# Optimization experiments

Hardware: AMD Instinct MI355X
Metric: run time of the kernel (lower is better)

The kernel has to match this reference:

```python
import jax, jax.numpy as jnp
import numpy as np
from jax import lax

VOCAB = 32000
D = 256      # d_model
N = 16       # n_neurons
NL = 6       # n_layers
DS = 16      # d_state
DC = 4       # d_conv
DI = 512     # d_inner = expand * d_model
DTR = 16     # dt_rank = ceil(D/16)
NH = 4       # attention heads
HD = D // NH
B, L = 1, 128


def setup_inputs() -> dict:
    key = jax.random.key(0)
    ks = list(jax.random.split(key, 32))
    it = iter(ks)

    def rn(shape, scale):
        return jax.random.normal(next(it), shape, jnp.float32) * scale

    p = {}
    p["x"] = jax.random.randint(next(it), (B, L), 0, VOCAB, dtype=jnp.int32)
    p["embedding"] = rn((VOCAB, D), 0.02)
    p["norm1_w"] = jnp.ones((NL, D)); p["norm1_b"] = jnp.zeros((NL, D))
    p["norm2_w"] = jnp.ones((NL, D)); p["norm2_b"] = jnp.zeros((NL, D))
    # Mamba params (stacked over layers)
    p["in_proj_w"] = rn((NL, 2 * DI, D), D ** -0.5)
    p["conv_w"] = rn((NL, DI, DC), DC ** -0.5)
    p["conv_b"] = jnp.zeros((NL, DI))
    p["x_proj_w"] = rn((NL, DTR + 2 * DS, DI), DI ** -0.5)
    p["dt_proj_w"] = rn((NL, DI, DTR), DTR ** -0.5)
    dt0 = jax.random.uniform(next(it), (NL, DI), jnp.float32, 1e-3, 1e-1)
    p["dt_proj_b"] = jnp.log(jnp.expm1(dt0))  # inverse softplus init
    p["A_log"] = jnp.log(jnp.tile(jnp.arange(1.0, DS + 1.0, dtype=jnp.float32), (NL, DI, 1)))
    p["skip_D"] = jnp.ones((NL, DI))
    p["out_proj_w"] = rn((NL, D, DI), DI ** -0.5)
    # cross-neuron MHA params
    p["attn_in_w"] = rn((NL, 3 * D, D), D ** -0.5)
    p["attn_in_b"] = jnp.zeros((NL, 3 * D))
    p["attn_out_w"] = rn((NL, D, D), D ** -0.5)
    p["attn_out_b"] = jnp.zeros((NL, D))
    p["norm_f_w"] = jnp.ones((D,)); p["norm_f_b"] = jnp.zeros((D,))
    p["head_b"] = jnp.zeros((VOCAB,))
    return p


def _ln(x, w, b):
    m = x.mean(-1, keepdims=True)
    v = ((x - m) ** 2).mean(-1, keepdims=True)
    return (x - m) * lax.rsqrt(v + 1e-5) * w + b


def _mamba(x, ipw, cw, cb, xpw, dpw, dpb, alog, dskip, opw):
    # x: (BN, L, D)
    BN, Ls, _ = x.shape
    xz = x @ ipw.T                       # (BN, L, 2*DI)
    u, z = xz[..., :DI], xz[..., DI:]
    # depthwise causal conv1d, kernel DC, left-pad DC-1
    uc = lax.conv_general_dilated(
        u.swapaxes(1, 2), cw[:, None, :], (1,), [(DC - 1, 0)],
        dimension_numbers=("NCH", "OIH", "NCH"), feature_group_count=DI)
    u = jax.nn.silu(uc + cb[None, :, None]).swapaxes(1, 2)  # (BN, L, DI)
    xdbl = u @ xpw.T                     # (BN, L, DTR+2*DS)
    dt = jax.nn.softplus(xdbl[..., :DTR] @ dpw.T + dpb)     # (BN, L, DI)
    Bm = xdbl[..., DTR:DTR + DS]
    Cm = xdbl[..., DTR + DS:]
    A = -jnp.exp(alog)                   # (DI, DS)

    def step(h, ins):
        dt_t, b_t, c_t, u_t = ins        # (BN,DI) (BN,DS) (BN,DS) (BN,DI)
        h = jnp.exp(dt_t[..., None] * A) * h + (dt_t * u_t)[..., None] * b_t[:, None, :]
        return h, jnp.einsum("bds,bs->bd", h, c_t)

    h0 = jnp.zeros((BN, DI, DS), x.dtype)
    _, ys = lax.scan(step, h0, (dt.swapaxes(0, 1), Bm.swapaxes(0, 1),
                                Cm.swapaxes(0, 1), u.swapaxes(0, 1)))
    y = ys.swapaxes(0, 1) + u * dskip
    return (y * jax.nn.silu(z)) @ opw.T


def _mha(x, iw, ib, ow, ob):
    # x: (B*L, N, D); self-attention across neurons
    Bq, S, _ = x.shape
    qkv = x @ iw.T + ib
    q, k, v = jnp.split(qkv, 3, axis=-1)
    q = q.reshape(Bq, S, NH, HD); k = k.reshape(Bq, S, NH, HD); v = v.reshape(Bq, S, NH, HD)
    att = jax.nn.softmax(jnp.einsum("bqhd,bkhd->bhqk", q, k) / np.float32(np.sqrt(HD)), axis=-1)
    o = jnp.einsum("bhqk,bkhd->bqhd", att, v).reshape(Bq, S, D)
    return o @ ow.T + ob


def reference(x, embedding, norm1_w, norm1_b, norm2_w, norm2_b, in_proj_w, conv_w,
              conv_b, x_proj_w, dt_proj_w, dt_proj_b, A_log, skip_D, out_proj_w,
              attn_in_w, attn_in_b, attn_out_w, attn_out_b, norm_f_w, norm_f_b, head_b):
    Bb, Ll = x.shape
    h = embedding[x]                                             # (B, L, D)
    h = jnp.broadcast_to(h[:, None], (Bb, N, Ll, D)).reshape(Bb * N, Ll, D)
    for i in range(NL):
        h = h + _mamba(_ln(h, norm1_w[i], norm1_b[i]), in_proj_w[i], conv_w[i],
                       conv_b[i], x_proj_w[i], dt_proj_w[i], dt_proj_b[i],
                       A_log[i], skip_D[i], out_proj_w[i])
        xc = _ln(h, norm2_w[i], norm2_b[i]).reshape(Bb, N, Ll, D)
        xc = xc.transpose(0, 2, 1, 3).reshape(Bb * Ll, N, D)
        co = _mha(xc, attn_in_w[i], attn_in_b[i], attn_out_w[i], attn_out_b[i])
        h = h + co.reshape(Bb, Ll, N, D).transpose(0, 2, 1, 3).reshape(Bb * N, Ll, D)
    h = h.reshape(Bb, N, Ll, D).mean(axis=1)                     # avg over neurons
    return _ln(h, norm_f_w, norm_f_b) @ embedding.T + head_b     # tied head
```

## Files before the change

kernel.cpp:

```cpp
#include <hip/hip_runtime.h>
#include <hip/hip_bf16.h>

typedef __bf16 bf16x8 __attribute__((ext_vector_type(8)));
typedef float f32x4 __attribute__((ext_vector_type(4)));

constexpr int SEQ    = 128;
constexpr int NVOCAB = 32000;

constexpr size_t O_HA = 0;
constexpr size_t O_HB = O_HA + (size_t)SEQ*256;
constexpr size_t O_U  = O_HB + (size_t)SEQ*256;
constexpr size_t O_DT = O_U  + (size_t)SEQ*512;
constexpr size_t O_ZS = O_DT + (size_t)SEQ*512;
constexpr size_t O_BC = O_ZS + (size_t)SEQ*512;
constexpr size_t O_YG = O_BC + (size_t)SEQ*32;
constexpr size_t O_AH = O_YG + (size_t)SEQ*512;
constexpr size_t O_EB = O_AH + (size_t)SEQ*256;

__device__ __forceinline__ float wsum(float p) {
    #pragma unroll
    for (int m = 1; m < 64; m <<= 1) p += __shfl_xor(p, m);
    return p;
}
__device__ __forceinline__ float dot4(float4 a, float4 b) {
    return a.x*b.x + a.y*b.y + a.z*b.z + a.w*b.w;
}

template<int MR, int KK>
__device__ __forceinline__ void gemmT(
    const float* __restrict__ Wg, const float* __restrict__ A, int AS,
    float* __restrict__ pb, float* __restrict__ dest, int DS,
    const float* __restrict__ addsrc, int ASS, const float* __restrict__ bias)
{
    const int tid  = threadIdx.x;
    const int lane = tid & 63;
    const int wv   = tid >> 6;
    const int kg   = wv >> 2;
    const int cg   = wv & 3;
    const int tq = lane & 3, cs = lane >> 2;
    const int c0 = cg*64 + cs*4;
    constexpr int KH  = KK/2;
    constexpr int NCH = KH/16;
    const int kb = kg*KH;
    const float* W0 = Wg + (size_t)(c0+0)*KK + kb + tq*4;
    const float* W1 = Wg + (size_t)(c0+1)*KK + kb + tq*4;
    const float* W2 = Wg + (size_t)(c0+2)*KK + kb + tq*4;
    const float* W3 = Wg + (size_t)(c0+3)*KK + kb + tq*4;

    float acc[MR][4];
    #pragma unroll
    for (int r = 0; r < MR; ++r)
        #pragma unroll
        for (int j = 0; j < 4; ++j) acc[r][j] = 0.0f;

    float4 e0 = *(const float4*)(W0);
    float4 e1 = *(const float4*)(W1);
    float4 e2 = *(const float4*)(W2);
    float4 e3 = *(const float4*)(W3);
    float4 o0, o1, o2, o3;

    #pragma unroll
    for (int ch = 0; ch < NCH; ch += 2) {
        o0 = *(const float4*)(W0 + (ch+1)*16);
        o1 = *(const float4*)(W1 + (ch+1)*16);
        o2 = *(const float4*)(W2 + (ch+1)*16);
        o3 = *(const float4*)(W3 + (ch+1)*16);
        #pragma unroll
        for (int r = 0; r < MR; ++r) {
            float4 a = *(const float4*)&A[r*AS + kb + ch*16 + tq*4];
            acc[r][0] += dot4(a, e0);
            acc[r][1] += dot4(a, e1);
            acc[r][2] += dot4(a, e2);
            acc[r][3] += dot4(a, e3);
        }
        if (ch + 2 < NCH) {
            e0 = *(const float4*)(W0 + (ch+2)*16);
            e1 = *(const float4*)(W1 + (ch+2)*16);
            e2 = *(const float4*)(W2 + (ch+2)*16);
            e3 = *(const float4*)(W3 + (ch+2)*16);
        }
        #pragma unroll
        for (int r = 0; r < MR; ++r) {
            float4 a = *(const float4*)&A[r*AS + kb + (ch+1)*16 + tq*4];
            acc[r][0] += dot4(a, o0);
            acc[r][1] += dot4(a, o1);
            acc[r][2] += dot4(a, o2);
            acc[r][3] += dot4(a, o3);
        }
    }
    #pragma unroll
    for (int r = 0; r < MR; ++r)
        #pragma unroll
        for (int j = 0; j < 4; ++j) {
            float v = acc[r][j];
            v += __shfl_xor(v, 1);
            v += __shfl_xor(v, 2);
            acc[r][j] = v;
        }
    if (tq == 0) {
        #pragma unroll
        for (int r = 0; r < MR; ++r)
            #pragma unroll
            for (int j = 0; j < 4; ++j)
                pb[(kg*MR + r)*256 + c0 + j] = acc[r][j];
    }
    __syncthreads();
    if (tid < 256) {
        int c = tid;
        #pragma unroll
        for (int r = 0; r < MR; ++r) {
            float v = pb[r*256 + c] + pb[(MR + r)*256 + c];
            if (bias)   v += bias[c];
            if (addsrc) v += addsrc[r*ASS + c];
            dest[r*DS + c] = v;
        }
    }
}

__device__ __forceinline__ void ln_row(const float* __restrict__ src, float* __restrict__ dst,
                                       const float* __restrict__ w, const float* __restrict__ b)
{
    int lane = threadIdx.x & 63;
    float4 x = *(const float4*)&src[lane*4];
    float sm = wsum(x.x + x.y + x.z + x.w);
    float mean = sm * (1.0f/256.0f);
    float d0 = x.x-mean, d1 = x.y-mean, d2 = x.z-mean, d3 = x.w-mean;
    float var = wsum(d0*d0 + d1*d1 + d2*d2 + d3*d3) * (1.0f/256.0f);
    float rstd = rsqrtf(var + 1e-5f);
    float4 ww = *(const float4*)&w[lane*4];
    float4 bb = *(const float4*)&b[lane*4];
    float4 o;
    o.x = d0*rstd*ww.x + bb.x;
    o.y = d1*rstd*ww.y + bb.y;
    o.z = d2*rstd*ww.z + bb.z;
    o.w = d3*rstd*ww.w + bb.w;
    *(float4*)&dst[lane*4] = o;
}

__global__ __launch_bounds__(256) void cvt_emb_kernel(const float* __restrict__ e,
                                                      __hip_bfloat16* __restrict__ o)
{
    size_t base = (size_t)(blockIdx.x * 256 + threadIdx.x) * 16;
    #pragma unroll
    for (int j = 0; j < 16; j += 4) {
        float4 v = *(const float4*)&e[base + j];
        o[base + j + 0] = __float2bfloat16(v.x);
        o[base + j + 1] = __float2bfloat16(v.y);
        o[base + j + 2] = __float2bfloat16(v.z);
        o[base + j + 3] = __float2bfloat16(v.w);
    }
}

__global__ __launch_bounds__(512) void rowk_kernel(
    const int* __restrict__ x, const float* __restrict__ emb,
    const float* __restrict__ n1w_l, const float* __restrict__ n1b_l,
    const float* __restrict__ n2w_l, const float* __restrict__ n2b_l,
    const float* __restrict__ ipw_l, const float* __restrict__ cw_l, const float* __restrict__ cb_l,
    const float* __restrict__ xpw_l, const float* __restrict__ dpw_l, const float* __restrict__ dpb_l,
    const float* __restrict__ opw_l, const float* __restrict__ aivw_l, const float* __restrict__ aivb_l,
    const float* __restrict__ aow_l, const float* __restrict__ aob_l,
    const float* __restrict__ nfw, const float* __restrict__ nfb,
    const float* __restrict__ hin, float* __restrict__ hout,
    const float* __restrict__ ygv, float* __restrict__ uv, float* __restrict__ dtv,
    float* __restrict__ zsv, float* __restrict__ bcv, __hip_bfloat16* __restrict__ AHb,
    int li)
{
    __shared__ float SM[8384];
    float* hP  = SM;
    float* h1  = SM + 1056;
    float* sLN = SM + 2112;
    float* sAX = SM + 3168;
    float* zR  = SM + 5248;
    float* suR = SM + 5760;
    float* sxR = SM + 6272;
    float* pb  = SM + 6336;

    const int r = blockIdx.x;
    const int tid = threadIdx.x;
    const int lane = tid & 63, wv = tid >> 6;
    int rr[4];
    #pragma unroll
    for (int j = 0; j < 4; ++j) { int v = r - 3 + j; rr[j] = v < 0 ? 0 : v; }

    #pragma unroll
    for (int j = 0; j < 2; ++j) {
        int idx = j*512 + tid;
        int hr = idx >> 8, hc = idx & 255;
        if (li <= 1) hP[hr*264 + hc] = emb[(size_t)x[rr[hr]]*256 + hc];
        else         hP[hr*264 + hc] = hin[rr[hr]*256 + hc];
    }
    __syncthreads();

    float* hC = hP;
    if (li >= 1) {
        #pragma unroll
        for (int j = 0; j < 4; ++j)
            sAX[j*520 + tid] = ygv[rr[j]*512 + tid];
        __syncthreads();
        gemmT<4,512>(opw_l, sAX, 520, pb, h1, 264, hP, 264, nullptr);
        __syncthreads();
        if (wv < 4) ln_row(h1 + wv*264, sLN + wv*264, n2w_l, n2b_l);
        __syncthreads();
        gemmT<4,256>(aivw_l, sLN, 264, pb, sAX, 520, nullptr, 0, aivb_l);
        __syncthreads();
        gemmT<4,256>(aow_l, sAX, 520, pb, h1, 264, h1, 264, aob_l);
        __syncthreads();
        hC = h1;
        if (tid < 256) hout[r*256 + tid] = h1[3*264 + tid];
        if (li == 6) {
            if (tid < 256) {
                float v = h1[3*264 + tid];
                float s = wsum(v);
                float q = wsum(v*v);
                if (lane == 0) { sxR[wv] = s; sxR[8 + wv] = q; }
            }
            __syncthreads();
            if (tid < 256) {
                float v = h1[3*264 + tid];
                float mean = (sxR[0]+sxR[1]+sxR[2]+sxR[3]) * (1.0f/256.0f);
                float var  = (sxR[8]+sxR[9]+sxR[10]+sxR[11]) * (1.0f/256.0f) - mean*mean;
                float rstd = rsqrtf(var + 1e-5f);
                AHb[r*256 + tid] = __float2bfloat16((v - mean)*rstd*nfw[tid] + nfb[tid]);
            }
            return;
        }
    }

    if (wv < 4) ln_row(hC + wv*264, sLN + wv*264, n1w_l, n1b_l);
    __syncthreads();
    gemmT<4,256>(ipw_l,                   sLN, 264, pb, sAX,       520, nullptr, 0, nullptr);
    __syncthreads();
    gemmT<4,256>(ipw_l + (size_t)256*256, sLN, 264, pb, sAX + 256, 520, nullptr, 0, nullptr);
    __syncthreads();
    gemmT<1,256>(ipw_l + (size_t)512*256, sLN + 3*264, 264, pb, zR,       512, nullptr, 0, nullptr);
    __syncthreads();
    gemmT<1,256>(ipw_l + (size_t)768*256, sLN + 3*264, 264, pb, zR + 256, 512, nullptr, 0, nullptr);
    __syncthreads();

    {
        int d = tid;
        float4 c4 = *(const float4*)&cw_l[d*4];
        float acc = cb_l[d];
        if (r >= 3) acc += sAX[d]        * c4.x;
        if (r >= 2) acc += sAX[520 + d]  * c4.y;
        if (r >= 1) acc += sAX[1040 + d] * c4.z;
        acc += sAX[1560 + d] * c4.w;
        float sg = acc / (1.0f + __expf(-acc));
        suR[d] = sg;
        uv[r*512 + d] = sg;
        float z = zR[d];
        zsv[r*512 + d] = z / (1.0f + __expf(-z));
    }
    __syncthreads();

    {
        float4 a0 = *(const float4*)&suR[lane*4];
        float4 a1 = *(const float4*)&suR[256 + lane*4];
        float p[6];
        #pragma unroll
        for (int j = 0; j < 6; ++j) {
            int c = wv*6 + j;
            float4 q0 = *(const float4*)&xpw_l[(size_t)c*512 + lane*4];
            float4 q1 = *(const float4*)&xpw_l[(size_t)c*512 + 256 + lane*4];
            p[j] = dot4(a0, q0) + dot4(a1, q1);
        }
        #pragma unroll
        for (int m = 1; m < 64; m <<= 1) {
            #pragma unroll
            for (int j = 0; j < 6; ++j) p[j] += __shfl_xor(p[j], m);
        }
        if (lane == 0) {
            #pragma unroll
            for (int j = 0; j < 6; ++j) sxR[wv*6 + j] = p[j];
        }
    }
    __syncthreads();
    if (tid >= 16 && tid < 48) bcv[r*32 + tid - 16] = sxR[tid];

    {
        int d = tid;
        float4 sx0 = *(const float4*)&sxR[0];
        float4 sx1 = *(const float4*)&sxR[4];
        float4 sx2 = *(const float4*)&sxR[8];
        float4 sx3 = *(const float4*)&sxR[12];
        const float4* dp = (const float4*)&dpw_l[(size_t)d*16];
        float acc = dpb_l[d] + dot4(dp[0], sx0) + dot4(dp[1], sx1)
                             + dot4(dp[2], sx2) + dot4(dp[3], sx3);
        dtv[r*512 + d] = fmaxf(acc, 0.0f) + log1pf(__expf(-fabsf(acc)));
    }
}

__global__ __launch_bounds__(256) void scan_kernel(
    const float* __restrict__ dt, const float* __restrict__ u, const float* __restrict__ zs,
    const float* __restrict__ bcv,
    const float* __restrict__ alog_l, const float* __restrict__ dsk_l,
    float* __restrict__ yg)
{
    __shared__ float s5[5*128];
    float* sdt = s5;        float* su2 = s5 + 128;
    float* sz2 = s5 + 256;  float* sB  = s5 + 384;  float* sC = s5 + 512;
    int tid = threadIdx.x;
    int s  = tid & 15, dl = tid >> 4;
    int d0 = blockIdx.x * 16;
    int d  = d0 + dl;
    float a_ds = -__expf(alog_l[d*16 + s]);
    float dskv = dsk_l[d];
    float hst = 0.0f;
    for (int t0 = 0; t0 < SEQ; t0 += 8) {
        __syncthreads();
        if (tid < 128) {
            int tt = tid >> 4, j = tid & 15;
            int t = t0 + tt;
            sdt[tt*16+j] = dt[t*512 + d0 + j];
            su2[tt*16+j] = u [t*512 + d0 + j];
            sz2[tt*16+j] = zs[t*512 + d0 + j];
        } else {
            int q = tid - 128;
            int tt = q >> 4, j = q & 15;
            int t = t0 + tt;
            sB[tt*16+j] = bcv[t*32 + j];
            sC[tt*16+j] = bcv[t*32 + 16 + j];
        }
        __syncthreads();
        #pragma unroll
        for (int tt = 0; tt < 8; ++tt) {
            float dtvv = sdt[tt*16+dl];
            float uvv  = su2[tt*16+dl];
            hst = __expf(dtvv * a_ds) * hst + dtvv * uvv * sB[tt*16+s];
            float p = hst * sC[tt*16+s];
            p += __shfl_xor(p, 1);
            p += __shfl_xor(p, 2);
            p += __shfl_xor(p, 4);
            p += __shfl_xor(p, 8);
            if (s == 0) {
                float y = p + uvv * dskv;
                yg[(t0+tt)*512 + d] = y * sz2[tt*16+dl];
            }
        }
    }
}

__global__ __launch_bounds__(256) void head_mfma_kernel(
    const __hip_bfloat16* __restrict__ AHb, const __hip_bfloat16* __restrict__ Eb,
    const float* __restrict__ hb, float* __restrict__ out)
{
    int tid = threadIdx.x;
    int lane = tid & 63;
    int wv = tid >> 6;
    int mbase = blockIdx.y * 16;
    int nbase = blockIdx.x * 64 + wv * 16;
    int m = mbase + (lane & 15);
    int n = nbase + (lane & 15);
    int k0 = (lane >> 4) * 8;
    const __bf16* Ap = (const __bf16*)AHb + m*256 + k0;
    const __bf16* Bp = (const __bf16*)Eb + (size_t)n*256 + k0;
    f32x4 acc = {0.0f, 0.0f, 0.0f, 0.0f};
    #pragma unroll
    for (int kb = 0; kb < 256; kb += 32) {
        bf16x8 a  = *(const bf16x8*)(Ap + kb);
        bf16x8 bb = *(const bf16x8*)(Bp + kb);
        acc = __builtin_amdgcn_mfma_f32_16x16x32_bf16(a, bb, acc, 0, 0, 0);
    }
    int col = lane & 15;
    int rq = lane >> 4;
    float bias = hb[nbase + col];
    #pragma unroll
    for (int i = 0; i < 4; ++i)
        out[(size_t)(mbase + rq*4 + i)*NVOCAB + nbase + col] = acc[i] + bias;
}

extern "C" void kernel_launch(void* const* d_in, const int* in_sizes, int n_in,
                              void* d_out, int out_size, void* d_ws, size_t ws_size,
                              hipStream_t stream)
{
    const int*   xin = (const int*)d_in[0];
    const float* emb = (const float*)d_in[1];
    const float* n1w = (const float*)d_in[2];
    const float* n1b = (const float*)d_in[3];
    const float* n2w = (const float*)d_in[4];
    const float* n2b = (const float*)d_in[5];
    const float* ipw = (const float*)d_in[6];
    const float* cw  = (const float*)d_in[7];
    const float* cb  = (const float*)d_in[8];
    const float* xpw = (const float*)d_in[9];
    const float* dpw = (const float*)d_in[10];
    const float* dpb = (const float*)d_in[11];
    const float* alog= (const float*)d_in[12];
    const float* dsk = (const float*)d_in[13];
    const float* opw = (const float*)d_in[14];
    const float* aiw = (const float*)d_in[15];
    const float* aib = (const float*)d_in[16];
    const float* aow = (const float*)d_in[17];
    const float* aob = (const float*)d_in[18];
    const float* nfw = (const float*)d_in[19];
    const float* nfb = (const float*)d_in[20];
    const float* hb  = (const float*)d_in[21];
    float* ws  = (float*)d_ws;
    float* out = (float*)d_out;

    __hip_bfloat16* AHb = (__hip_bfloat16*)(ws + O_AH);
    __hip_bfloat16* Eb  = (__hip_bfloat16*)(ws + O_EB);

    cvt_emb_kernel<<<2000, 256, 0, stream>>>(emb, Eb);

    for (int i = 0; i <= 6; ++i) {
        int ka = i <= 5 ? i : 5;
        int kc = i >= 1 ? i - 1 : 0;
        const float* hin  = (i % 2 == 0) ? ws + O_HA : ws + O_HB;
        float*       hout = (i % 2 == 0) ? ws + O_HB : ws + O_HA;
        rowk_kernel<<<128, 512, 0, stream>>>(
            xin, emb,
            n1w + ka*256, n1b + ka*256,
            n2w + kc*256, n2b + kc*256,
            ipw + (size_t)ka*1024*256, cw + (size_t)ka*512*4, cb + ka*512,
            xpw + (size_t)ka*48*512, dpw + (size_t)ka*512*16, dpb + ka*512,
            opw + (size_t)kc*256*512,
            aiw + (size_t)kc*768*256 + (size_t)512*256, aib + kc*768 + 512,
            aow + (size_t)kc*256*256, aob + kc*256,
            nfw, nfb,
            hin, hout,
            ws + O_YG, ws + O_U, ws + O_DT, ws + O_ZS, ws + O_BC, AHb,
            i);
        if (i <= 5)
            scan_kernel<<<32, 256, 0, stream>>>(
                ws + O_DT, ws + O_U, ws + O_ZS, ws + O_BC,
                alog + (size_t)i*512*16, dsk + i*512, ws + O_YG);
    }
    head_mfma_kernel<<<dim3(NVOCAB/64, SEQ/16), 256, 0, stream>>>(AHb, Eb, hb, out);
}
```

Before: 671.1 us.

## Convert per-row layer GEMMs to bf16 MFMA with pre-converted weights

Result: faster. 601.4 us (-10.4%).

```diff
diff --git a/kernel.cpp b/kernel.cpp
--- a/kernel.cpp
+++ b/kernel.cpp
@@ -3,6 +3,7 @@
 
 typedef __bf16 bf16x8 __attribute__((ext_vector_type(8)));
 typedef float f32x4 __attribute__((ext_vector_type(4)));
+typedef __hip_bfloat16 hbf;
 
 constexpr int SEQ    = 128;
 constexpr int NVOCAB = 32000;
@@ -16,6 +17,10 @@
 constexpr size_t O_YG = O_BC + (size_t)SEQ*32;
 constexpr size_t O_AH = O_YG + (size_t)SEQ*512;
 constexpr size_t O_EB = O_AH + (size_t)SEQ*256;
+constexpr size_t O_WIP= O_EB + (size_t)NVOCAB*256/2;
+constexpr size_t O_WOP= O_WIP+ (size_t)6*1024*256/2;
+constexpr size_t O_WAV= O_WOP+ (size_t)6*256*512/2;
+constexpr size_t O_WAO= O_WAV+ (size_t)6*256*256/2;
 
 __device__ __forceinline__ float wsum(float p) {
     #pragma unroll
@@ -26,99 +31,54 @@
     return a.x*b.x + a.y*b.y + a.z*b.z + a.w*b.w;
 }
 
-template<int MR, int KK>
-__device__ __forceinline__ void gemmT(
-    const float* __restrict__ Wg, const float* __restrict__ A, int AS,
-    float* __restrict__ pb, float* __restrict__ dest, int DS,
+template<int KK, int NT, bool R3>
+__device__ __forceinline__ void gemmM(
+    const hbf* __restrict__ Wb, const hbf* __restrict__ Ab, int ASb,
+    float* __restrict__ dest, int DS, hbf* __restrict__ destb, int DSB,
     const float* __restrict__ addsrc, int ASS, const float* __restrict__ bias)
 {
-    const int tid  = threadIdx.x;
-    const int lane = tid & 63;
-    const int wv   = tid >> 6;
-    const int kg   = wv >> 2;
-    const int cg   = wv & 3;
-    const int tq = lane & 3, cs = lane >> 2;
-    const int c0 = cg*64 + cs*4;
-    constexpr int KH  = KK/2;
-    constexpr int NCH = KH/16;
-    const int kb = kg*KH;
-    const float* W0 = Wg + (size_t)(c0+0)*KK + kb + tq*4;
-    const float* W1 = Wg + (size_t)(c0+1)*KK + kb + tq*4;
-    const float* W2 = Wg + (size_t)(c0+2)*KK + kb + tq*4;
-    const float* W3 = Wg + (size_t)(c0+3)*KK + kb + tq*4;
-
-    float acc[MR][4];
-    #pragma unroll
-    for (int r = 0; r < MR; ++r)
-        #pragma unroll
-        for (int j = 0; j < 4; ++j) acc[r][j] = 0.0f;
-
-    float4 e0 = *(const float4*)(W0);
-    float4 e1 = *(const float4*)(W1);
-    float4 e2 = *(const float4*)(W2);
-    float4 e3 = *(const float4*)(W3);
-    float4 o0, o1, o2, o3;
-
-    #pragma unroll
-    for (int ch = 0; ch < NCH; ch += 2) {
-        o0 = *(const float4*)(W0 + (ch+1)*16);
-        o1 = *(const float4*)(W1 + (ch+1)*16);
-        o2 = *(const float4*)(W2 + (ch+1)*16);
-        o3 = *(const float4*)(W3 + (ch+1)*16);
-        #pragma unroll
-        for (int r = 0; r < MR; ++r) {
-            float4 a = *(const float4*)&A[r*AS + kb + ch*16 + tq*4];
-            acc[r][0] += dot4(a, e0);
-            acc[r][1] += dot4(a, e1);
-            acc[r][2] += dot4(a, e2);
-            acc[r][3] += dot4(a, e3);
-        }
-        if (ch + 2 < NCH) {
-            e0 = *(const float4*)(W0 + (ch+2)*16);
-            e1 = *(const float4*)(W1 + (ch+2)*16);
-            e2 = *(const float4*)(W2 + (ch+2)*16);
-            e3 = *(const float4*)(W3 + (ch+2)*16);
-        }
-        #pragma unroll
-        for (int r = 0; r < MR; ++r) {
-            float4 a = *(const float4*)&A[r*AS + kb + (ch+1)*16 + tq*4];
-            acc[r][0] += dot4(a, o0);
-            acc[r][1] += dot4(a, o1);
-            acc[r][2] += dot4(a, o2);
-            acc[r][3] += dot4(a, o3);
-        }
-    }
-    #pragma unroll
-    for (int r = 0; r < MR; ++r)
-        #pragma unroll
-        for (int j = 0; j < 4; ++j) {
-            float v = acc[r][j];
-            v += __shfl_xor(v, 1);
-            v += __shfl_xor(v, 2);
-            acc[r][j] = v;
-        }
-    if (tq == 0) {
-        #pragma unroll
-        for (int r = 0; r < MR; ++r)
+    constexpr int TPW = NT/128;
+    constexpr int NCH = KK/32;
+    const int lane = threadIdx.x & 63;
+    const int wv   = threadIdx.x >> 6;
+    const int col  = lane & 15;
+    const int kq   = lane >> 4;
+    const __bf16* Ap = (const __bf16*)Ab + (lane & 3)*ASb + kq*8;
+    const __bf16* Wp = (const __bf16*)Wb + (size_t)(wv*TPW*16 + col)*KK + kq*8;
+    f32x4 acc[TPW];
+    #pragma unroll
+    for (int t = 0; t < TPW; ++t) acc[t] = (f32x4){0.f,0.f,0.f,0.f};
+    #pragma unroll
+    for (int ch = 0; ch < NCH; ++ch) {
+        bf16x8 a = *(const bf16x8*)(Ap + ch*32);
+        #pragma unroll
+        for (int t = 0; t < TPW; ++t) {
+            bf16x8 b = *(const bf16x8*)(Wp + (size_t)t*16*KK + ch*32);
+            acc[t] = __builtin_amdgcn_mfma_f32_16x16x32_bf16(a, b, acc[t], 0, 0, 0);
+        }
+    }
+    if (lane < 16) {
+        #pragma unroll
+        for (int t = 0; t < TPW; ++t) {
+            int c = (wv*TPW + t)*16 + col;
+            float bv = bias ? bias[c] : 0.0f;
             #pragma unroll
-            for (int j = 0; j < 4; ++j)
-                pb[(kg*MR + r)*256 + c0 + j] = acc[r][j];
-    }
-    __syncthreads();
-    if (tid < 256) {
-        int c = tid;
-        #pragma unroll
-        for (int r = 0; r < MR; ++r) {
-            float v = pb[r*256 + c] + pb[(MR + r)*256 + c];
-            if (bias)   v += bias[c];
-            if (addsrc) v += addsrc[r*ASS + c];
-            dest[r*DS + c] = v;
-        }
-    }
-}
-
-__device__ __forceinline__ void ln_row(const float* __restrict__ src, float* __restrict__ dst,
-                                       const float* __restrict__ w, const float* __restrict__ b)
+            for (int i = 0; i < 4; ++i) {
+                float v = acc[t][i] + bv;
+                if (addsrc) v += addsrc[i*ASS + c];
+                if (R3) {
+                    if (i == 3) dest[c] = v;
+                } else {
+                    if (dest)  dest[i*DS + c] = v;
+                    if (destb) destb[i*DSB + c] = __float2bfloat16(v);
+                }
+            }
+        }
+    }
+}
+
+__device__ __forceinline__ void ln_row_b(const float* __restrict__ src, hbf* __restrict__ dstb,
+                                         const float* __restrict__ w, const float* __restrict__ b)
 {
     int lane = threadIdx.x & 63;
     float4 x = *(const float4*)&src[lane*4];
@@ -129,16 +89,14 @@
     float rstd = rsqrtf(var + 1e-5f);
     float4 ww = *(const float4*)&w[lane*4];
     float4 bb = *(const float4*)&b[lane*4];
-    float4 o;
-    o.x = d0*rstd*ww.x + bb.x;
-    o.y = d1*rstd*ww.y + bb.y;
-    o.z = d2*rstd*ww.z + bb.z;
-    o.w = d3*rstd*ww.w + bb.w;
-    *(float4*)&dst[lane*4] = o;
+    dstb[lane*4+0] = __float2bfloat16(d0*rstd*ww.x + bb.x);
+    dstb[lane*4+1] = __float2bfloat16(d1*rstd*ww.y + bb.y);
+    dstb[lane*4+2] = __float2bfloat16(d2*rstd*ww.z + bb.z);
+    dstb[lane*4+3] = __float2bfloat16(d3*rstd*ww.w + bb.w);
 }
 
 __global__ __launch_bounds__(256) void cvt_emb_kernel(const float* __restrict__ e,
-                                                      __hip_bfloat16* __restrict__ o)
+                                                      hbf* __restrict__ o)
 {
     size_t base = (size_t)(blockIdx.x * 256 + threadIdx.x) * 16;
     #pragma unroll
@@ -151,29 +109,49 @@
     }
 }
 
+__global__ __launch_bounds__(256) void cvt_w_kernel(
+    const float* __restrict__ ipw, const float* __restrict__ opw,
+    const float* __restrict__ aiw, const float* __restrict__ aow,
+    float* __restrict__ ws)
+{
+    hbf* dip = (hbf*)(ws + O_WIP);
+    hbf* dop = (hbf*)(ws + O_WOP);
+    hbf* dav = (hbf*)(ws + O_WAV);
+    hbf* dao = (hbf*)(ws + O_WAO);
+    int tid = blockIdx.x * 256 + threadIdx.x;
+    int stride = gridDim.x * 256;
+    for (int i = tid; i < 6*1024*256; i += stride) dip[i] = __float2bfloat16(ipw[i]);
+    for (int i = tid; i < 6*256*512;  i += stride) dop[i] = __float2bfloat16(opw[i]);
+    for (int i = tid; i < 6*256*256;  i += stride)
+        dav[i] = __float2bfloat16(aiw[(size_t)(i >> 16)*768*256 + 512*256 + (i & 65535)]);
+    for (int i = tid; i < 6*256*256;  i += stride) dao[i] = __float2bfloat16(aow[i]);
+}
+
 __global__ __launch_bounds__(512) void rowk_kernel(
     const int* __restrict__ x, const float* __restrict__ emb,
     const float* __restrict__ n1w_l, const float* __restrict__ n1b_l,
     const float* __restrict__ n2w_l, const float* __restrict__ n2b_l,
-    const float* __restrict__ ipw_l, const float* __restrict__ cw_l, const float* __restrict__ cb_l,
+    const hbf* __restrict__ ipb_l, const float* __restrict__ cw_l, const float* __restrict__ cb_l,
     const float* __restrict__ xpw_l, const float* __restrict__ dpw_l, const float* __restrict__ dpb_l,
-    const float* __restrict__ opw_l, const float* __restrict__ aivw_l, const float* __restrict__ aivb_l,
-    const float* __restrict__ aow_l, const float* __restrict__ aob_l,
+    const hbf* __restrict__ opb_l, const hbf* __restrict__ avb_l, const float* __restrict__ aivb_l,
+    const hbf* __restrict__ aob_wl, const float* __restrict__ aob_l,
     const float* __restrict__ nfw, const float* __restrict__ nfb,
     const float* __restrict__ hin, float* __restrict__ hout,
     const float* __restrict__ ygv, float* __restrict__ uv, float* __restrict__ dtv,
-    float* __restrict__ zsv, float* __restrict__ bcv, __hip_bfloat16* __restrict__ AHb,
+    float* __restrict__ zsv, float* __restrict__ bcv, hbf* __restrict__ AHb,
     int li)
 {
-    __shared__ float SM[8384];
+    __shared__ float SM[5280];
     float* hP  = SM;
     float* h1  = SM + 1056;
-    float* sLN = SM + 2112;
-    float* sAX = SM + 3168;
-    float* zR  = SM + 5248;
-    float* suR = SM + 5760;
-    float* sxR = SM + 6272;
-    float* pb  = SM + 6336;
+    float* sAX = SM + 2112;
+    float* zR  = SM + 4192;
+    float* suR = SM + 4704;
+    float* sxR = SM + 5216;
+    __shared__ __align__(16) hbf SB[4192];
+    hbf* sYb  = SB;
+    hbf* sLNb = SB + 2080;
+    hbf* sVb  = SB + 3136;
 
     const int r = blockIdx.x;
     const int tid = threadIdx.x;
@@ -195,15 +173,15 @@
     if (li >= 1) {
         #pragma unroll
         for (int j = 0; j < 4; ++j)
-            sAX[j*520 + tid] = ygv[rr[j]*512 + tid];
-        __syncthreads();
-        gemmT<4,512>(opw_l, sAX, 520, pb, h1, 264, hP, 264, nullptr);
-        __syncthreads();
-        if (wv < 4) ln_row(h1 + wv*264, sLN + wv*264, n2w_l, n2b_l);
-        __syncthreads();
-        gemmT<4,256>(aivw_l, sLN, 264, pb, sAX, 520, nullptr, 0, aivb_l);
-        __syncthreads();
-        gemmT<4,256>(aow_l, sAX, 520, pb, h1, 264, h1, 264, aob_l);
+            sYb[j*520 + tid] = __float2bfloat16(ygv[rr[j]*512 + tid]);
+        __syncthreads();
+        gemmM<512,256,false>(opb_l, sYb, 520, h1, 264, nullptr, 0, hP, 264, nullptr);
+        __syncthreads();
+        if (wv < 4) ln_row_b(h1 + wv*264, sLNb + wv*264, n2w_l, n2b_l);
+        __syncthreads();
+        gemmM<256,256,false>(avb_l, sLNb, 264, nullptr, 0, sVb, 264, nullptr, 0, aivb_l);
+        __syncthreads();
+        gemmM<256,256,false>(aob_wl, sVb, 264, h1, 264, nullptr, 0, h1, 264, aob_l);
         __syncthreads();
         hC = h1;
         if (tid < 256) hout[r*256 + tid] = h1[3*264 + tid];
@@ -226,15 +204,10 @@
         }
     }
 
-    if (wv < 4) ln_row(hC + wv*264, sLN + wv*264, n1w_l, n1b_l);
+    if (wv < 4) ln_row_b(hC + wv*264, sLNb + wv*264, n1w_l, n1b_l);
     __syncthreads();
-    gemmT<4,256>(ipw_l,                   sLN, 264, pb, sAX,       520, nullptr, 0, nullptr);
-    __syncthreads();
-    gemmT<4,256>(ipw_l + (size_t)256*256, sLN, 264, pb, sAX + 256, 520, nullptr, 0, nullptr);
-    __syncthreads();
-    gemmT<1,256>(ipw_l + (size_t)512*256, sLN + 3*264, 264, pb, zR,       512, nullptr, 0, nullptr);
-    __syncthreads();
-    gemmT<1,256>(ipw_l + (size_t)768*256, sLN + 3*264, 264, pb, zR + 256, 512, nullptr, 0, nullptr);
+    gemmM<256,512,false>(ipb_l,                   sLNb, 264, sAX, 520, nullptr, 0, nullptr, 0, nullptr);
+    gemmM<256,512,true >(ipb_l + (size_t)512*256, sLNb, 264, zR,  0,   nullptr, 0, nullptr, 0, nullptr);
     __syncthreads();
 
     {
@@ -341,7 +314,7 @@
 }
 
 __global__ __launch_bounds__(256) void head_mfma_kernel(
-    const __hip_bfloat16* __restrict__ AHb, const __hip_bfloat16* __restrict__ Eb,
+    const hbf* __restrict__ AHb, const hbf* __restrict__ Eb,
     const float* __restrict__ hb, float* __restrict__ out)
 {
     int tid = threadIdx.x;
@@ -398,10 +371,11 @@
     float* ws  = (float*)d_ws;
     float* out = (float*)d_out;
 
-    __hip_bfloat16* AHb = (__hip_bfloat16*)(ws + O_AH);
-    __hip_bfloat16* Eb  = (__hip_bfloat16*)(ws + O_EB);
+    hbf* AHb = (hbf*)(ws + O_AH);
+    hbf* Eb  = (hbf*)(ws + O_EB);
 
     cvt_emb_kernel<<<2000, 256, 0, stream>>>(emb, Eb);
+    cvt_w_kernel<<<1024, 256, 0, stream>>>(ipw, opw, aiw, aow, ws);
 
     for (int i = 0; i <= 6; ++i) {
         int ka = i <= 5 ? i : 5;
@@ -412,11 +386,12 @@
             xin, emb,
             n1w + ka*256, n1b + ka*256,
             n2w + kc*256, n2b + kc*256,
-            ipw + (size_t)ka*1024*256, cw + (size_t)ka*512*4, cb + ka*512,
+            (hbf*)(ws + O_WIP) + (size_t)ka*1024*256,
+            cw + (size_t)ka*512*4, cb + ka*512,
             xpw + (size_t)ka*48*512, dpw + (size_t)ka*512*16, dpb + ka*512,
-            opw + (size_t)kc*256*512,
-            aiw + (size_t)kc*768*256 + (size_t)512*256, aib + kc*768 + 512,
-            aow + (size_t)kc*256*256, aob + kc*256,
+            (hbf*)(ws + O_WOP) + (size_t)kc*256*512,
+            (hbf*)(ws + O_WAV) + (size_t)kc*256*256, aib + kc*768 + 512,
+            (hbf*)(ws + O_WAO) + (size_t)kc*256*256, aob + kc*256,
             nfw, nfb,
             hin, hout,
             ws + O_YG, ws + O_U, ws + O_DT, ws + O_ZS, ws + O_BC, AHb,
```
